# Performance work log

Hardware: AMD Instinct MI355X
Metric: run time of the kernel (lower is better)

## Reference

```python
import jax, jax.numpy as jnp
import numpy as np

VOCAB, EMBED, HIDDEN, LAYERS = 32000, 512, 1024, 2
BATCH, SEQ = 32, 128


def gru_layer(x_tbe, h0, W_ih, W_hh, b_ih, b_hh):
    """x_tbe: [T,B,E_in]; h0: [B,H]. PyTorch GRU gate math."""
    # Precompute input-side gates for all timesteps (one big GEMM).
    gi = jnp.einsum('tbe,ge->tbg', x_tbe, W_ih) + b_ih  # [T,B,3H]

    def step(h, gi_t):
        gh = h @ W_hh.T + b_hh                      # [B,3H]
        i_r, i_z, i_n = jnp.split(gi_t, 3, axis=-1)
        h_r, h_z, h_n = jnp.split(gh, 3, axis=-1)
        r = jax.nn.sigmoid(i_r + h_r)
        z = jax.nn.sigmoid(i_z + h_z)
        n = jnp.tanh(i_n + r * h_n)
        h_new = (1.0 - z) * n + z * h
        return h_new, h_new

    hT, ys = jax.lax.scan(step, h0, gi)
    return ys, hT  # ys: [T,B,H]


def setup_inputs() -> dict:
    key = jax.random.key(0)
    ks = jax.random.split(key, 16)
    s = 0.02
    inp = {
        'inputs': jax.random.randint(ks[0], (BATCH, SEQ), 0, VOCAB),
        'lengths': jax.random.randint(ks[1], (BATCH,), 1, SEQ),
        'hidden': jax.random.normal(ks[2], (LAYERS, BATCH, HIDDEN), jnp.float32),
        'embed_table': jax.random.normal(ks[3], (VOCAB, EMBED), jnp.float32) * s,
        'W_ih_l0': jax.random.normal(ks[4], (3 * HIDDEN, EMBED), jnp.float32) * s,
        'W_hh_l0': jax.random.normal(ks[5], (3 * HIDDEN, HIDDEN), jnp.float32) * s,
        'b_ih_l0': jnp.zeros((3 * HIDDEN,), jnp.float32),
        'b_hh_l0': jnp.zeros((3 * HIDDEN,), jnp.float32),
        'W_ih_l1': jax.random.normal(ks[6], (3 * HIDDEN, HIDDEN), jnp.float32) * s,
        'W_hh_l1': jax.random.normal(ks[7], (3 * HIDDEN, HIDDEN), jnp.float32) * s,
        'b_ih_l1': jnp.zeros((3 * HIDDEN,), jnp.float32),
        'b_hh_l1': jnp.zeros((3 * HIDDEN,), jnp.float32),
        'W_out': jax.random.normal(ks[8], (VOCAB, HIDDEN), jnp.float32) * s,
        'b_out': jnp.zeros((VOCAB,), jnp.float32),
    }
    return inp


def reference(inputs, lengths, hidden, embed_table,
              W_ih_l0, W_hh_l0, b_ih_l0, b_hh_l0,
              W_ih_l1, W_hh_l1, b_ih_l1, b_hh_l1,
              W_out, b_out):
    # embedding: [B,S,E] -> time-major [S,B,E]
    x = embed_table[inputs].transpose(1, 0, 2)
    x, _ = gru_layer(x, hidden[0], W_ih_l0, W_hh_l0, b_ih_l0, b_hh_l0)
    x, _ = gru_layer(x, hidden[1], W_ih_l1, W_hh_l1, b_ih_l1, b_hh_l1)
    outputs = x.transpose(1, 0, 2)                   # [B,S,H]
    logits = outputs @ W_out.T + b_out               # [B,S,V]
    return logits
```

## Files before the change

kernel.cpp:

```cpp
#include <hip/hip_runtime.h>
#include <hip/hip_bf16.h>
#include <stdint.h>

#define T_SEQ 128
#define NBATCH 32
#define EMBED 512
#define HID 1024
#define NVOCAB 32000

typedef float f32x4 __attribute__((ext_vector_type(4)));
typedef _Float16 f16x8 __attribute__((ext_vector_type(8)));

__device__ __forceinline__ unsigned short f2h(float f) {
  _Float16 h = (_Float16)f;
  return __builtin_bit_cast(unsigned short, h);
}
__device__ __forceinline__ float sigm(float x) {
  return 1.0f / (1.0f + __expf(-x));
}
__device__ __forceinline__ float tanh_fast(float x) {
  return 2.0f / (1.0f + __expf(-2.0f * x)) - 1.0f;
}
__device__ __forceinline__ unsigned umin4(unsigned a, unsigned b, unsigned c, unsigned d) {
  unsigned x = a < b ? a : b;
  unsigned y = c < d ? c : d;
  return x < y ? x : y;
}

__global__ void k_zero(unsigned int* __restrict__ p, int n) {
  int i = blockIdx.x * blockDim.x + threadIdx.x;
  if (i < n) p[i] = 0;
}

__global__ void k_f32_to_f16(const float4* __restrict__ in,
                             ushort4* __restrict__ out, int n4) {
  int i = blockIdx.x * blockDim.x + threadIdx.x;
  int stride = gridDim.x * blockDim.x;
  for (; i < n4; i += stride) {
    float4 v = in[i];
    ushort4 o;
    o.x = f2h(v.x); o.y = f2h(v.y); o.z = f2h(v.z); o.w = f2h(v.w);
    out[i] = o;
  }
}

__global__ void k_embed(const int* __restrict__ tok, const float* __restrict__ table,
                        ushort4* __restrict__ A0) {
  int tid = blockIdx.x * 256 + threadIdx.x;
  int m = tid >> 7, kq = tid & 127;
  int b = m & 31, t = m >> 5;
  int tk = tok[b * T_SEQ + t];
  float4 v = *(const float4*)(table + (size_t)tk * EMBED + kq * 4);
  ushort4 o;
  o.x = f2h(v.x); o.y = f2h(v.y); o.z = f2h(v.z); o.w = f2h(v.w);
  A0[tid] = o;
}

#define BM 128
#define BN 128
#define BKK 64

__global__ __launch_bounds__(256) void k_gemm_bt(
    const short* __restrict__ A,
    const short* __restrict__ B,
    float* __restrict__ C,
    const float* __restrict__ bias,
    int M, int N, int K, int permute)
{
  __shared__ __align__(16) short As[BM * BKK];
  __shared__ __align__(16) short Bs[BN * BKK];
  const int tid = threadIdx.x;
  const int w = tid >> 6, l = tid & 63;
  const int wr = w >> 1, wc = w & 1;
  const int bm = blockIdx.x * BM, bn = blockIdx.y * BN;
  const int l15 = l & 15, lkg = l >> 4;

  f32x4 acc[4][4] = {};

  for (int kt = 0; kt < K; kt += BKK) {
#pragma unroll
    for (int p = 0; p < 4; ++p) {
      int idx = p * 2048 + tid * 8;
      int r = idx >> 6, c = idx & 63;
      *(f16x8*)&As[idx] = *(const f16x8*)&A[(size_t)(bm + r) * K + kt + c];
      *(f16x8*)&Bs[idx] = *(const f16x8*)&B[(size_t)(bn + r) * K + kt + c];
    }
    __syncthreads();

#pragma unroll
    for (int ks = 0; ks < 2; ++ks) {
      f16x8 af[4], bfr[4];
#pragma unroll
      for (int mi = 0; mi < 4; ++mi)
        af[mi] = *(const f16x8*)&As[(wr * 64 + mi * 16 + l15) * BKK + ks * 32 + lkg * 8];
#pragma unroll
      for (int ni = 0; ni < 4; ++ni)
        bfr[ni] = *(const f16x8*)&Bs[(wc * 64 + ni * 16 + l15) * BKK + ks * 32 + lkg * 8];
#pragma unroll
      for (int mi = 0; mi < 4; ++mi)
#pragma unroll
        for (int ni = 0; ni < 4; ++ni)
          acc[mi][ni] = __builtin_amdgcn_mfma_f32_16x16x32_f16(
              af[mi], bfr[ni], acc[mi][ni], 0, 0, 0);
    }
    __syncthreads();
  }

  const int lr = lkg * 4;
#pragma unroll
  for (int mi = 0; mi < 4; ++mi) {
#pragma unroll
    for (int ni = 0; ni < 4; ++ni) {
      int col = bn + wc * 64 + ni * 16 + l15;
      float bv = bias ? bias[col] : 0.0f;
#pragma unroll
      for (int j = 0; j < 4; ++j) {
        int row = bm + wr * 64 + mi * 16 + lr + j;
        int orow = permute ? ((row & 31) * T_SEQ + (row >> 5)) : row;
        C[(size_t)orow * N + col] = acc[mi][ni][j] + bv;
      }
    }
  }
}

__global__ __launch_bounds__(384, 2) void k_gru_fused(
    const float* __restrict__ gi0,
    const float* __restrict__ Whh0,
    const float* __restrict__ bhh0,
    const float* __restrict__ Wih1,
    const float* __restrict__ bih1,
    const float* __restrict__ Whh1,
    const float* __restrict__ bhh1,
    const _Float16* __restrict__ h0i,
    const _Float16* __restrict__ h1i,
    _Float16* __restrict__ ys0f,
    _Float16* __restrict__ ys1f,
    unsigned int* flg0,
    unsigned int* flg1)
{
  __shared__ float bufIH[2][3][2][64];

  const int tid = threadIdx.x;
  const int l = tid & 63;
  const int w = tid >> 6;
  const int role = w >> 1, nt = w & 1;
  const int bid = blockIdx.x;
  const int j0 = bid * 4;

  const int row16 = l & 15;
  const int jjr = row16 >> 2, gate = row16 & 3;
  const int koct = l >> 4;

  const int b_out = nt * 16 + (l & 15);
  const int j_out = j0 + (l >> 4);
  const int jj_even = (((l >> 4) & 1) == 0);

  const float* Wsrc = (role == 0) ? Whh0 : ((role == 1) ? Wih1 : Whh1);
  f16x8 af[32];
  if (gate < 3) {
    const float* wrow = Wsrc + (size_t)(gate * HID + j0 + jjr) * HID;
#pragma unroll
    for (int c = 0; c < 32; ++c) {
      float4 p0 = *(const float4*)(wrow + c * 32 + koct * 8);
      float4 p1 = *(const float4*)(wrow + c * 32 + koct * 8 + 4);
      f16x8 v = { (_Float16)p0.x, (_Float16)p0.y, (_Float16)p0.z, (_Float16)p0.w,
                  (_Float16)p1.x, (_Float16)p1.y, (_Float16)p1.z, (_Float16)p1.w };
      af[c] = v;
    }
  } else {
#pragma unroll
    for (int c = 0; c < 32; ++c) {
      f16x8 z = { (_Float16)0.f, (_Float16)0.f, (_Float16)0.f, (_Float16)0.f,
                  (_Float16)0.f, (_Float16)0.f, (_Float16)0.f, (_Float16)0.f };
      af[c] = z;
    }
  }

  float bR = 0.f, bZ = 0.f, bN = 0.f, biR = 0.f, biZ = 0.f, biN = 0.f;
  if (role == 0) {
    bR = bhh0[j_out]; bZ = bhh0[HID + j_out]; bN = bhh0[2 * HID + j_out];
  } else if (role == 2) {
    bR = bhh1[j_out]; bZ = bhh1[HID + j_out]; bN = bhh1[2 * HID + j_out];
    biR = bih1[j_out]; biZ = bih1[HID + j_out]; biN = bih1[2 * HID + j_out];
  }

  const int bfragOff = b_out * 2048 + koct * 16;

  for (int s = 0; s <= T_SEQ + 1; ++s) {
    float pre_ir = 0.f, pre_iz = 0.f, pre_in = 0.f;
    if (role == 0 && s < T_SEQ) {
      const float* gib = gi0 + (size_t)(s * NBATCH + b_out) * 3072 + j_out;
      pre_ir = gib[0]; pre_iz = gib[HID]; pre_in = gib[2 * HID];
    }

    if (w == 0) {
      unsigned need0 = (s >= 1 && s <= T_SEQ) ? (unsigned)s : 0u;
      unsigned need1 = (s >= 3) ? (unsigned)(s - 2) : 0u;
      if ((need0 | need1) != 0u) {
        const unsigned* f0 = flg0 + l * 4;
        const unsigned* f1 = flg1 + l * 4;
        for (;;) {
          unsigned m0 = 0xffffffffu, m1 = 0xffffffffu;
          if (need0) {
            unsigned a0 = __hip_atomic_load(f0 + 0, __ATOMIC_RELAXED, __HIP_MEMORY_SCOPE_AGENT);
            unsigned a1 = __hip_atomic_load(f0 + 1, __ATOMIC_RELAXED, __HIP_MEMORY_SCOPE_AGENT);
            unsigned a2 = __hip_atomic_load(f0 + 2, __ATOMIC_RELAXED, __HIP_MEMORY_SCOPE_AGENT);
            unsigned a3 = __hip_atomic_load(f0 + 3, __ATOMIC_RELAXED, __HIP_MEMORY_SCOPE_AGENT);
            m0 = umin4(a0, a1, a2, a3);
          }
          if (need1) {
            unsigned a0 = __hip_atomic_load(f1 + 0, __ATOMIC_RELAXED, __HIP_MEMORY_SCOPE_AGENT);
            unsigned a1 = __hip_atomic_load(f1 + 1, __ATOMIC_RELAXED, __HIP_MEMORY_SCOPE_AGENT);
            unsigned a2 = __hip_atomic_load(f1 + 2, __ATOMIC_RELAXED, __HIP_MEMORY_SCOPE_AGENT);
            unsigned a3 = __hip_atomic_load(f1 + 3, __ATOMIC_RELAXED, __HIP_MEMORY_SCOPE_AGENT);
            m1 = umin4(a0, a1, a2, a3);
          }
          if (__all(m0 >= need0 && m1 >= need1)) break;
          __builtin_amdgcn_s_sleep(1);
        }
        asm volatile("" ::: "memory");
      }
    }
    __syncthreads();

    if (role == 0 && s < T_SEQ) {
      const _Float16* hsrc = (s == 0) ? h0i : (ys0f + (size_t)(s - 1) * NBATCH * HID);
      const char* hb = (const char*)hsrc + bfragOff;
      f32x4 acc0 = {}, acc1 = {};
#pragma unroll
      for (int c = 0; c < 32; c += 2) {
        f16x8 bf0 = *(const f16x8*)(hb + c * 64);
        f16x8 bf1 = *(const f16x8*)(hb + c * 64 + 64);
        acc0 = __builtin_amdgcn_mfma_f32_16x16x32_f16(af[c], bf0, acc0, 0, 0, 0);
        acc1 = __builtin_amdgcn_mfma_f32_16x16x32_f16(af[c + 1], bf1, acc1, 0, 0, 0);
      }
      f32x4 acc = acc0 + acc1;

      float hp = (float)((s == 0) ? h0i[b_out * HID + j_out]
                                  : ys0f[(size_t)((s - 1) * NBATCH + b_out) * HID + j_out]);
      float r = sigm(pre_ir + acc[0] + bR);
      float z = sigm(pre_iz + acc[1] + bZ);
      float n = tanh_fast(pre_in + r * (acc[2] + bN));
      float hnew = (1.0f - z) * n + z * hp;

      unsigned bits = (unsigned)f2h(hnew);
      unsigned hi = __shfl_down(bits, 16);
      if (jj_even) {
        unsigned packed = (bits & 0xffffu) | (hi << 16);
        __hip_atomic_store((unsigned*)(ys0f + (size_t)(s * NBATCH + b_out) * HID + j_out),
                           packed, __ATOMIC_RELAXED, __HIP_MEMORY_SCOPE_AGENT);
      }
    }

    if (role == 1 && s >= 1 && s <= T_SEQ) {
      const _Float16* hsrc = ys0f + (size_t)(s - 1) * NBATCH * HID;
      const char* hb = (const char*)hsrc + bfragOff;
      f32x4 acc0 = {}, acc1 = {};
#pragma unroll
      for (int c = 0; c < 32; c += 2) {
        f16x8 bf0 = *(const f16x8*)(hb + c * 64);
        f16x8 bf1 = *(const f16x8*)(hb + c * 64 + 64);
        acc0 = __builtin_amdgcn_mfma_f32_16x16x32_f16(af[c], bf0, acc0, 0, 0, 0);
        acc1 = __builtin_amdgcn_mfma_f32_16x16x32_f16(af[c + 1], bf1, acc1, 0, 0, 0);
      }
      f32x4 acc = acc0 + acc1;
      bufIH[s & 1][0][nt][l] = acc[0];
      bufIH[s & 1][1][nt][l] = acc[1];
      bufIH[s & 1][2][nt][l] = acc[2];
    }

    if (role == 2 && s >= 2) {
      const int t1 = s - 2;
      const _Float16* hsrc = (t1 == 0) ? h1i : (ys1f + (size_t)(t1 - 1) * NBATCH * HID);
      const char* hb = (const char*)hsrc + bfragOff;
      f32x4 acc0 = {}, acc1 = {};
#pragma unroll
      for (int c = 0; c < 32; c += 2) {
        f16x8 bf0 = *(const f16x8*)(hb + c * 64);
        f16x8 bf1 = *(const f16x8*)(hb + c * 64 + 64);
        acc0 = __builtin_amdgcn_mfma_f32_16x16x32_f16(af[c], bf0, acc0, 0, 0, 0);
        acc1 = __builtin_amdgcn_mfma_f32_16x16x32_f16(af[c + 1], bf1, acc1, 0, 0, 0);
      }
      f32x4 acc = acc0 + acc1;

      const int par = (s - 1) & 1;
      float ihR = bufIH[par][0][nt][l] + biR;
      float ihZ = bufIH[par][1][nt][l] + biZ;
      float ihN = bufIH[par][2][nt][l] + biN;
      float hp = (float)((t1 == 0) ? h1i[b_out * HID + j_out]
                                   : ys1f[(size_t)((t1 - 1) * NBATCH + b_out) * HID + j_out]);
      float r = sigm(ihR + acc[0] + bR);
      float z = sigm(ihZ + acc[1] + bZ);
      float n = tanh_fast(ihN + r * (acc[2] + bN));
      float hnew = (1.0f - z) * n + z * hp;

      unsigned bits = (unsigned)f2h(hnew);
      unsigned hi = __shfl_down(bits, 16);
      if (jj_even) {
        unsigned packed = (bits & 0xffffu) | (hi << 16);
        __hip_atomic_store((unsigned*)(ys1f + (size_t)(t1 * NBATCH + b_out) * HID + j_out),
                           packed, __ATOMIC_RELAXED, __HIP_MEMORY_SCOPE_AGENT);
      }
    }

    __syncthreads();

    if (tid == 0) {
      if (s < T_SEQ)
        __hip_atomic_store(&flg0[bid], (unsigned)(s + 1), __ATOMIC_RELAXED, __HIP_MEMORY_SCOPE_AGENT);
      if (s >= 2)
        __hip_atomic_store(&flg1[bid], (unsigned)(s - 1), __ATOMIC_RELAXED, __HIP_MEMORY_SCOPE_AGENT);
    }
  }
}

extern "C" void kernel_launch(void* const* d_in, const int* in_sizes, int n_in,
                              void* d_out, int out_size, void* d_ws, size_t ws_size,
                              hipStream_t stream)
{
  const int*   inputs = (const int*)d_in[0];
  const float* hidden = (const float*)d_in[2];
  const float* table  = (const float*)d_in[3];
  const float* Wih0   = (const float*)d_in[4];
  const float* Whh0   = (const float*)d_in[5];
  const float* bih0   = (const float*)d_in[6];
  const float* bhh0   = (const float*)d_in[7];
  const float* Wih1   = (const float*)d_in[8];
  const float* Whh1   = (const float*)d_in[9];
  const float* bih1   = (const float*)d_in[10];
  const float* bhh1   = (const float*)d_in[11];
  const float* Wout   = (const float*)d_in[12];
  const float* bout   = (const float*)d_in[13];
  float* out = (float*)d_out;

  char* ws = (char*)d_ws;
  size_t off = 0;
  auto alloc = [&](size_t bytes) {
    void* p = ws + off;
    off += (bytes + 255) & ~(size_t)255;
    return p;
  };
  float*     gi0  = (float*)alloc((size_t)4096 * 3072 * 4);
  _Float16*  ys0f = (_Float16*)alloc((size_t)4096 * 1024 * 2);
  _Float16*  ys1f = (_Float16*)alloc((size_t)4096 * 1024 * 2);
  short*     A0   = (short*)alloc((size_t)4096 * 512 * 2);
  short*     B0   = (short*)alloc((size_t)3072 * 512 * 2);
  short*     B2   = (short*)alloc((size_t)32000 * 1024 * 2);
  _Float16*  hcat = (_Float16*)alloc((size_t)2 * 32 * 1024 * 2);
  _Float16*  h0i  = hcat;
  _Float16*  h1i  = hcat + 32 * 1024;
  unsigned int* flg0 = (unsigned int*)alloc(256 * 4);
  unsigned int* flg1 = (unsigned int*)alloc(256 * 4);

  k_zero<<<1, 512, 0, stream>>>(flg0, 512);

  k_f32_to_f16<<<1024, 256, 0, stream>>>((const float4*)Wih0, (ushort4*)B0, 3072 * 512 / 4);
  k_f32_to_f16<<<2048, 256, 0, stream>>>((const float4*)Wout, (ushort4*)B2, 32000 * 1024 / 4);
  k_f32_to_f16<<<64, 256, 0, stream>>>((const float4*)hidden, (ushort4*)hcat, 2 * 32 * 1024 / 4);
  k_embed<<<2048, 256, 0, stream>>>(inputs, table, (ushort4*)A0);

  dim3 g0(32, 24);
  k_gemm_bt<<<g0, 256, 0, stream>>>(A0, B0, gi0, bih0, 4096, 3072, 512, 0);

  {
    void* kargs[] = {
      (void*)&gi0, (void*)&Whh0, (void*)&bhh0,
      (void*)&Wih1, (void*)&bih1, (void*)&Whh1, (void*)&bhh1,
      (void*)&h0i, (void*)&h1i, (void*)&ys0f, (void*)&ys1f,
      (void*)&flg0, (void*)&flg1
    };
    hipLaunchCooperativeKernel((const void*)k_gru_fused, dim3(256), dim3(384),
                               kargs, 0, stream);
  }

  dim3 g2(32, 250);
  k_gemm_bt<<<g2, 256, 0, stream>>>((const short*)ys1f, B2, out, bout, 4096, 32000, 1024, 1);
}
```

Measured before the change: 1.581 ms.

## Replace all-to-all flag polling with block-0 aggregator and per-role epoch flags

Instead of every block polling all 256 per-block flags each step, block 0 alone aggregates per-wave flags and publishes replicated epoch counters, which other blocks poll with a single load. Producer waves now publish their own flags right after their stores, which removes the end-of-step __syncthreads, and each role waits only for the dependency it actually needs. This cuts cross-CU polling traffic and barrier latency, at the cost of an extra hop through the aggregator block on the critical path. It also adds a non-cooperative launch fallback.

```diff
diff --git a/kernel.cpp b/kernel.cpp
--- a/kernel.cpp
+++ b/kernel.cpp
@@ -7,6 +7,7 @@
 #define EMBED 512
 #define HID 1024
 #define NVOCAB 32000
+#define NBLK 256
 
 typedef float f32x4 __attribute__((ext_vector_type(4)));
 typedef _Float16 f16x8 __attribute__((ext_vector_type(8)));
@@ -20,11 +21,6 @@
 }
 __device__ __forceinline__ float tanh_fast(float x) {
   return 2.0f / (1.0f + __expf(-2.0f * x)) - 1.0f;
-}
-__device__ __forceinline__ unsigned umin4(unsigned a, unsigned b, unsigned c, unsigned d) {
-  unsigned x = a < b ? a : b;
-  unsigned y = c < d ? c : d;
-  return x < y ? x : y;
 }
 
 __global__ void k_zero(unsigned int* __restrict__ p, int n) {
@@ -136,15 +132,17 @@
     _Float16* __restrict__ ys0f,
     _Float16* __restrict__ ys1f,
     unsigned int* flg0,
-    unsigned int* flg1)
+    unsigned int* flg1,
+    unsigned int* epoch0,
+    unsigned int* epoch1)
 {
   __shared__ float bufIH[2][3][2][64];
 
   const int tid = threadIdx.x;
   const int l = tid & 63;
   const int w = tid >> 6;
+  const int bid = blockIdx.x;
   const int role = w >> 1, nt = w & 1;
-  const int bid = blockIdx.x;
   const int j0 = bid * 4;
 
   const int row16 = l & 15;
@@ -186,6 +184,9 @@
 
   const int bfragOff = b_out * 2048 + koct * 16;
 
+  const unsigned* ep0 = epoch0 + (bid & 7) * 64;
+  const unsigned* ep1 = epoch1 + (bid & 7) * 64;
+
   for (int s = 0; s <= T_SEQ + 1; ++s) {
     float pre_ir = 0.f, pre_iz = 0.f, pre_in = 0.f;
     if (role == 0 && s < T_SEQ) {
@@ -193,29 +194,51 @@
       pre_ir = gib[0]; pre_iz = gib[HID]; pre_in = gib[2 * HID];
     }
 
-    if (w == 0) {
-      unsigned need0 = (s >= 1 && s <= T_SEQ) ? (unsigned)s : 0u;
-      unsigned need1 = (s >= 3) ? (unsigned)(s - 2) : 0u;
-      if ((need0 | need1) != 0u) {
-        const unsigned* f0 = flg0 + l * 4;
-        const unsigned* f1 = flg1 + l * 4;
+    if (bid == 0) {
+      if (w == 0) {
+        unsigned need0 = (s >= 1 && s <= T_SEQ) ? (unsigned)s : 0u;
+        unsigned need1 = (s >= 3) ? (unsigned)(s - 2) : 0u;
+        if ((need0 | need1) != 0u) {
+          const unsigned* f0 = flg0 + l * 8;
+          const unsigned* f1 = flg1 + l * 8;
+          for (;;) {
+            unsigned m0 = 0xffffffffu, m1 = 0xffffffffu;
+            if (need0) {
+#pragma unroll
+              for (int i = 0; i < 8; ++i) {
+                unsigned v = __hip_atomic_load(f0 + i, __ATOMIC_RELAXED, __HIP_MEMORY_SCOPE_AGENT);
+                m0 = v < m0 ? v : m0;
+              }
+            }
+            if (need1) {
+#pragma unroll
+              for (int i = 0; i < 8; ++i) {
+                unsigned v = __hip_atomic_load(f1 + i, __ATOMIC_RELAXED, __HIP_MEMORY_SCOPE_AGENT);
+                m1 = v < m1 ? v : m1;
+              }
+            }
+            if (__all(m0 >= need0 && m1 >= need1)) break;
+            __builtin_amdgcn_s_sleep(1);
+          }
+          if (l < 8) {
+            if (need0)
+              __hip_atomic_store(epoch0 + l * 64, need0, __ATOMIC_RELAXED, __HIP_MEMORY_SCOPE_AGENT);
+            if (need1)
+              __hip_atomic_store(epoch1 + l * 64, need1, __ATOMIC_RELAXED, __HIP_MEMORY_SCOPE_AGENT);
+          }
+          asm volatile("" ::: "memory");
+        }
+      }
+    } else {
+      unsigned need = 0;
+      const unsigned* ep = ep0;
+      if (role == 0) { if (s >= 1 && s < T_SEQ)  need = (unsigned)s; }
+      else if (role == 1) { if (s >= 1 && s <= T_SEQ) need = (unsigned)s; }
+      else { if (s >= 3) { need = (unsigned)(s - 2); ep = ep1; } }
+      if (need) {
         for (;;) {
-          unsigned m0 = 0xffffffffu, m1 = 0xffffffffu;
-          if (need0) {
-            unsigned a0 = __hip_atomic_load(f0 + 0, __ATOMIC_RELAXED, __HIP_MEMORY_SCOPE_AGENT);
-            unsigned a1 = __hip_atomic_load(f0 + 1, __ATOMIC_RELAXED, __HIP_MEMORY_SCOPE_AGENT);
-            unsigned a2 = __hip_atomic_load(f0 + 2, __ATOMIC_RELAXED, __HIP_MEMORY_SCOPE_AGENT);
-            unsigned a3 = __hip_atomic_load(f0 + 3, __ATOMIC_RELAXED, __HIP_MEMORY_SCOPE_AGENT);
-            m0 = umin4(a0, a1, a2, a3);
-          }
-          if (need1) {
-            unsigned a0 = __hip_atomic_load(f1 + 0, __ATOMIC_RELAXED, __HIP_MEMORY_SCOPE_AGENT);
-            unsigned a1 = __hip_atomic_load(f1 + 1, __ATOMIC_RELAXED, __HIP_MEMORY_SCOPE_AGENT);
-            unsigned a2 = __hip_atomic_load(f1 + 2, __ATOMIC_RELAXED, __HIP_MEMORY_SCOPE_AGENT);
-            unsigned a3 = __hip_atomic_load(f1 + 3, __ATOMIC_RELAXED, __HIP_MEMORY_SCOPE_AGENT);
-            m1 = umin4(a0, a1, a2, a3);
-          }
-          if (__all(m0 >= need0 && m1 >= need1)) break;
+          unsigned e = __hip_atomic_load(ep, __ATOMIC_RELAXED, __HIP_MEMORY_SCOPE_AGENT);
+          if (e >= need) break;
           __builtin_amdgcn_s_sleep(1);
         }
         asm volatile("" ::: "memory");
@@ -250,6 +273,10 @@
         __hip_atomic_store((unsigned*)(ys0f + (size_t)(s * NBATCH + b_out) * HID + j_out),
                            packed, __ATOMIC_RELAXED, __HIP_MEMORY_SCOPE_AGENT);
       }
+      asm volatile("s_waitcnt vmcnt(0)" ::: "memory");
+      if (l == 0)
+        __hip_atomic_store(&flg0[bid * 2 + nt], (unsigned)(s + 1),
+                           __ATOMIC_RELAXED, __HIP_MEMORY_SCOPE_AGENT);
     }
 
     if (role == 1 && s >= 1 && s <= T_SEQ) {
@@ -301,15 +328,10 @@
         __hip_atomic_store((unsigned*)(ys1f + (size_t)(t1 * NBATCH + b_out) * HID + j_out),
                            packed, __ATOMIC_RELAXED, __HIP_MEMORY_SCOPE_AGENT);
       }
-    }
-
-    __syncthreads();
-
-    if (tid == 0) {
-      if (s < T_SEQ)
-        __hip_atomic_store(&flg0[bid], (unsigned)(s + 1), __ATOMIC_RELAXED, __HIP_MEMORY_SCOPE_AGENT);
-      if (s >= 2)
-        __hip_atomic_store(&flg1[bid], (unsigned)(s - 1), __ATOMIC_RELAXED, __HIP_MEMORY_SCOPE_AGENT);
+      asm volatile("s_waitcnt vmcnt(0)" ::: "memory");
+      if (l == 0)
+        __hip_atomic_store(&flg1[bid * 2 + nt], (unsigned)(s - 1),
+                           __ATOMIC_RELAXED, __HIP_MEMORY_SCOPE_AGENT);
     }
   }
 }
@@ -349,10 +371,12 @@
   _Float16*  hcat = (_Float16*)alloc((size_t)2 * 32 * 1024 * 2);
   _Float16*  h0i  = hcat;
   _Float16*  h1i  = hcat + 32 * 1024;
-  unsigned int* flg0 = (unsigned int*)alloc(256 * 4);
-  unsigned int* flg1 = (unsigned int*)alloc(256 * 4);
-
-  k_zero<<<1, 512, 0, stream>>>(flg0, 512);
+  unsigned int* flg0   = (unsigned int*)alloc(512 * 4);
+  unsigned int* flg1   = (unsigned int*)alloc(512 * 4);
+  unsigned int* epoch0 = (unsigned int*)alloc(512 * 4);
+  unsigned int* epoch1 = (unsigned int*)alloc(512 * 4);
+
+  k_zero<<<8, 256, 0, stream>>>(flg0, 2048);
 
   k_f32_to_f16<<<1024, 256, 0, stream>>>((const float4*)Wih0, (ushort4*)B0, 3072 * 512 / 4);
   k_f32_to_f16<<<2048, 256, 0, stream>>>((const float4*)Wout, (ushort4*)B2, 32000 * 1024 / 4);
@@ -367,10 +391,16 @@
       (void*)&gi0, (void*)&Whh0, (void*)&bhh0,
       (void*)&Wih1, (void*)&bih1, (void*)&Whh1, (void*)&bhh1,
       (void*)&h0i, (void*)&h1i, (void*)&ys0f, (void*)&ys1f,
-      (void*)&flg0, (void*)&flg1
+      (void*)&flg0, (void*)&flg1, (void*)&epoch0, (void*)&epoch1
     };
-    hipLaunchCooperativeKernel((const void*)k_gru_fused, dim3(256), dim3(384),
-                               kargs, 0, stream);
+    hipError_t e = hipLaunchCooperativeKernel((const void*)k_gru_fused, dim3(NBLK),
+                                              dim3(384), kargs, 0, stream);
+    if (e != hipSuccess) {
+      (void)hipGetLastError();
+      k_gru_fused<<<dim3(NBLK), dim3(384), 0, stream>>>(
+          gi0, Whh0, bhh0, Wih1, bih1, Whh1, bhh1,
+          h0i, h1i, ys0f, ys1f, flg0, flg1, epoch0, epoch1);
+    }
   }
 
   dim3 g2(32, 250);
```

Result: slower. 1.802 ms (+14.0%).

## Replace output projection GEMM with 256x256-tile double-buffered direct-to-LDS kernel

Applied to the files above, without the earlier changes.

Adds a new fp16 MFMA GEMM for the vocab projection that uses 256x256 block tiles, 512 threads, global_load_lds staging into swizzled double-buffered LDS, and phased prefetch of the next K tiles interleaved with MFMA quads under raised wave priority. It replaces the generic 128-tile GEMM for the 4096x32000x1024 output layer, aiming for more data reuse per block and better overlap of loads and math. It also adds a fallback to a normal launch if the cooperative launch fails. The large tile and 128 KB of LDS per block limit occupancy, and 32000 is an exact multiple of 256 so no edge handling is needed.

```diff
diff --git a/kernel.cpp b/kernel.cpp
--- a/kernel.cpp
+++ b/kernel.cpp
@@ -7,6 +7,7 @@
 #define EMBED 512
 #define HID 1024
 #define NVOCAB 32000
+#define NBLK 256
 
 typedef float f32x4 __attribute__((ext_vector_type(4)));
 typedef _Float16 f16x8 __attribute__((ext_vector_type(8)));
@@ -117,6 +118,143 @@
       for (int j = 0; j < 4; ++j) {
         int row = bm + wr * 64 + mi * 16 + lr + j;
         int orow = permute ? ((row & 31) * T_SEQ + (row >> 5)) : row;
+        C[(size_t)orow * N + col] = acc[mi][ni][j] + bv;
+      }
+    }
+  }
+}
+
+#define LK 1024
+#define GNT 16
+
+__global__ __launch_bounds__(512, 2) void k_gemm256(
+    const short* __restrict__ A,
+    const short* __restrict__ B,
+    float* __restrict__ C,
+    const float* __restrict__ bias,
+    int N)
+{
+  __shared__ __align__(16) short As[2][256 * 64];
+  __shared__ __align__(16) short Bs[2][256 * 64];
+
+  const int tid = threadIdx.x;
+  const int l = tid & 63, wid = tid >> 6;
+  const int wm = wid >> 2, wn = wid & 3;
+  const int l15 = l & 15, lkg = l >> 4;
+  const int bm = blockIdx.x * 256, bn = blockIdx.y * 256;
+
+  f32x4 acc[8][4] = {};
+
+  auto stage_half = [&](int kt, int op, int half) {
+    const short* G = op ? B : A;
+    const int base_row = (op ? bn : bm) + half * 128;
+    char* L = (char*)(op ? Bs[kt & 1] : As[kt & 1]) + half * 128 * 64 * 2;
+#pragma unroll
+    for (int p = 0; p < 2; ++p) {
+      int chunk = p * 512 + tid;
+      int Lbyte = chunk * 16;
+      int r = Lbyte >> 7;
+      int cb = Lbyte & 127;
+      int scb = cb ^ ((r & 7) << 4);
+      const char* src = (const char*)&G[(size_t)(base_row + r) * LK + kt * 64] + scb;
+      char* dst = L + (p * 512 + wid * 64) * 16;
+      __builtin_amdgcn_global_load_lds(
+          (const __attribute__((address_space(1))) void*)src,
+          (__attribute__((address_space(3))) void*)dst, 16, 0, 0);
+    }
+  };
+
+  stage_half(0, 0, 0); stage_half(0, 0, 1);
+  stage_half(0, 1, 0); stage_half(0, 1, 1);
+  stage_half(1, 0, 0); stage_half(1, 0, 1);
+  asm volatile("s_waitcnt vmcnt(4)" ::: "memory");
+  __builtin_amdgcn_sched_barrier(0);
+  __builtin_amdgcn_s_barrier();
+  __builtin_amdgcn_sched_barrier(0);
+
+  for (int kt = 0; kt < GNT; ++kt) {
+    const char* bufA = (const char*)As[kt & 1];
+    const char* bufB = (const char*)Bs[kt & 1];
+    f16x8 afr[8][2];
+    f16x8 bfr[2][2];
+
+#define RD_A(mi_, ks_) \
+    (*(const f16x8*)(bufA + ((wm * 128 + (mi_) * 16 + l15) * 128 + \
+        (((ks_) * 64 + lkg * 16) ^ (((wm * 128 + (mi_) * 16 + l15) & 7) << 4)))))
+#define RD_B(ni_, ks_) \
+    (*(const f16x8*)(bufB + ((wn * 64 + (ni_) * 16 + l15) * 128 + \
+        (((ks_) * 64 + lkg * 16) ^ (((wn * 64 + (ni_) * 16 + l15) & 7) << 4)))))
+
+#define MFMA_QUAD(MI0, NI0) \
+    __builtin_amdgcn_s_setprio(1); \
+    _Pragma("unroll") \
+    for (int ks = 0; ks < 2; ++ks) \
+      _Pragma("unroll") \
+      for (int i = 0; i < 4; ++i) \
+        _Pragma("unroll") \
+        for (int j = 0; j < 2; ++j) \
+          acc[(MI0) + i][(NI0) + j] = __builtin_amdgcn_mfma_f32_16x16x32_f16( \
+              afr[(MI0) + i][ks], bfr[j][ks], acc[(MI0) + i][(NI0) + j], 0, 0, 0); \
+    __builtin_amdgcn_s_setprio(0);
+
+#define PHASE_BARS() \
+    __builtin_amdgcn_s_barrier(); __builtin_amdgcn_sched_barrier(0);
+
+#pragma unroll
+    for (int i = 0; i < 4; ++i) { afr[i][0] = RD_A(i, 0); afr[i][1] = RD_A(i, 1); }
+#pragma unroll
+    for (int j = 0; j < 2; ++j) { bfr[j][0] = RD_B(j, 0); bfr[j][1] = RD_B(j, 1); }
+    if (kt + 1 < GNT) stage_half(kt + 1, 1, 0);
+    PHASE_BARS();
+    MFMA_QUAD(0, 0);
+    PHASE_BARS();
+
+#pragma unroll
+    for (int i = 0; i < 4; ++i) { afr[4 + i][0] = RD_A(4 + i, 0); afr[4 + i][1] = RD_A(4 + i, 1); }
+    if (kt + 1 < GNT) stage_half(kt + 1, 1, 1);
+    PHASE_BARS();
+    MFMA_QUAD(4, 0);
+    PHASE_BARS();
+
+#pragma unroll
+    for (int j = 0; j < 2; ++j) { bfr[j][0] = RD_B(2 + j, 0); bfr[j][1] = RD_B(2 + j, 1); }
+    if (kt + 2 < GNT) stage_half(kt + 2, 0, 0);
+    PHASE_BARS();
+    MFMA_QUAD(0, 2);
+    PHASE_BARS();
+
+    if (kt + 2 < GNT) stage_half(kt + 2, 0, 1);
+    PHASE_BARS();
+    MFMA_QUAD(4, 2);
+    PHASE_BARS();
+
+    if (kt + 1 < GNT) {
+      if (kt + 2 < GNT) {
+        asm volatile("s_waitcnt vmcnt(4)" ::: "memory");
+      } else {
+        asm volatile("s_waitcnt vmcnt(0)" ::: "memory");
+      }
+      __builtin_amdgcn_sched_barrier(0);
+      __builtin_amdgcn_s_barrier();
+      __builtin_amdgcn_sched_barrier(0);
+    }
+#undef RD_A
+#undef RD_B
+#undef MFMA_QUAD
+#undef PHASE_BARS
+  }
+
+  const int lr = lkg * 4;
+#pragma unroll
+  for (int mi = 0; mi < 8; ++mi) {
+#pragma unroll
+    for (int ni = 0; ni < 4; ++ni) {
+      int col = bn + wn * 64 + ni * 16 + l15;
+      float bv = bias[col];
+#pragma unroll
+      for (int j = 0; j < 4; ++j) {
+        int row = bm + wm * 128 + mi * 16 + lr + j;
+        int orow = (row & 31) * T_SEQ + (row >> 5);
         C[(size_t)orow * N + col] = acc[mi][ni][j] + bv;
       }
     }
@@ -369,10 +507,16 @@
       (void*)&h0i, (void*)&h1i, (void*)&ys0f, (void*)&ys1f,
       (void*)&flg0, (void*)&flg1
     };
-    hipLaunchCooperativeKernel((const void*)k_gru_fused, dim3(256), dim3(384),
-                               kargs, 0, stream);
-  }
-
-  dim3 g2(32, 250);
-  k_gemm_bt<<<g2, 256, 0, stream>>>((const short*)ys1f, B2, out, bout, 4096, 32000, 1024, 1);
-}
+    hipError_t e = hipLaunchCooperativeKernel((const void*)k_gru_fused, dim3(NBLK),
+                                              dim3(384), kargs, 0, stream);
+    if (e != hipSuccess) {
+      (void)hipGetLastError();
+      k_gru_fused<<<dim3(NBLK), dim3(384), 0, stream>>>(
+          gi0, Whh0, bhh0, Wih1, bih1, Whh1, bhh1,
+          h0i, h1i, ys0f, ys1f, flg0, flg1);
+    }
+  }
+
+  dim3 g2(16, 125);
+  k_gemm256<<<g2, 512, 0, stream>>>((const short*)ys1f, B2, out, bout, NVOCAB);
+}
```

After: 1.470 ms. 7.0% less time.
